# Optimization experiments

Hardware: AMD Instinct MI355X
Metric: run time of the kernel (lower is better)

Reference implementation:

```python
import jax, jax.numpy as jnp
import numpy as np

FS = 44100
N_SINES = 1000
RESAMPLE = 32
TWO_PI = 2.0 * np.pi


def _linear_upsample(x, scale):
    """Match torch F.interpolate(mode='linear', align_corners=False).
    x: [B, C, N] -> [B, C, N*scale]"""
    n = x.shape[-1]
    out_n = n * scale
    # source coordinate for each output sample
    coords = (jnp.arange(out_n, dtype=jnp.float32) + 0.5) / scale - 0.5
    coords = jnp.clip(coords, 0.0, n - 1)
    lo = jnp.floor(coords).astype(jnp.int32)
    hi = jnp.minimum(lo + 1, n - 1)
    w = (coords - lo.astype(jnp.float32)).astype(x.dtype)
    return x[..., lo] * (1.0 - w) + x[..., hi] * w


def setup_inputs() -> dict:
    key = jax.random.key(0)
    k1, k2 = jax.random.split(key)
    B, S, F = 4, N_SINES, 256
    frequencies = jax.random.uniform(k1, (B, S, F), dtype=jnp.float32) * 5000.0 + 40.0
    amplitudes = jax.random.uniform(k2, (B, S, F), dtype=jnp.float32) / N_SINES
    init_phases = jnp.zeros((B, S), dtype=jnp.float32)
    return {"frequencies": frequencies, "amplitudes": amplitudes, "init_phases": init_phases}


def reference(frequencies, amplitudes, init_phases):
    freqs = _linear_upsample(frequencies, RESAMPLE)
    amps = _linear_upsample(amplitudes, RESAMPLE)
    # angular increment per sample
    omegas = freqs * (TWO_PI / FS)
    # phase accumulation (inclusive cumsum) plus carried-in phase state
    phases = jnp.cumsum(omegas, axis=-1) + init_phases[:, :, None]
    # additive synthesis: sum over sines -> [B, 1, T]
    signal = jnp.sum(amps * jnp.sin(phases), axis=1, keepdims=True)
    return signal
```

## Files before the change

### kernel.cpp

```cpp
#include <hip/hip_runtime.h>


#define FS_D 44100.0
#define S_TOTAL 1000
#define FRAMES 256
#define T_OUT 8192
#define BATCH 4
#define CH 8
#define NC 125
#define KQ 4

template <bool ATOMIC>
__global__ __launch_bounds__(256) void synth(
    const float* __restrict__ freq, const float* __restrict__ amp,
    const float* __restrict__ initp, float* __restrict__ dst)
{
  __shared__ float base_lds[CH][FRAMES];
  __shared__ float head_lds[CH];

  const int bx    = blockIdx.x;
  const int b     = bx / (NC * KQ);
  const int rem   = bx % (NC * KQ);
  const int chunk = rem >> 2;
  const int kq    = rem & 3;
  const int s0    = chunk * CH;
  const int tid   = threadIdx.x;
  const int lane  = tid & 63;
  const int wave  = tid >> 6;

  const double inv2pi = 0.15915494309189535;
  const double k16    = 16.0 / FS_D;

  #pragma unroll
  for (int r = wave; r < CH; r += 4) {
    const int s = s0 + r;
    const long long roff = (long long)(b * S_TOTAL + s) * FRAMES;
    const float4 fv = reinterpret_cast<const float4*>(freq + roff)[lane];
    const double f0 = fv.x, f1 = fv.y, f2 = fv.z, f3 = fv.w;
    const double tot = f0 + f1 + f2 + f3;
    double incl = tot;
    #pragma unroll
    for (int off = 1; off < 64; off <<= 1) {
      double v = __shfl_up(incl, (unsigned)off, 64);
      if (lane >= off) incl += v;
    }
    double C = incl - tot;
    const double initrev = (double)initp[b * S_TOTAL + s] * inv2pi;
    if (lane == 0) head_lds[r] = (float)(initrev - floor(initrev));
    const double fk[4] = {f0, f1, f2, f3};
    #pragma unroll
    for (int i = 0; i < 4; ++i) {
      const double basev = k16 * (2.0 * C + fk[i]) + initrev;
      base_lds[r][4 * lane + i] = (float)(basev - floor(basev));
      C += fk[i];
    }
  }
  __syncthreads();

  const int g = tid >> 2;
  const int q = tid & 3;
  const int k = kq * 64 + g;
  const bool special = (k == 255);
  const bool hd      = special && (q >= 2);
  const int kA  = hd ? 0 : k;
  const int kA1 = special ? kA : (kA + 1);
  const int qq  = hd ? (q - 2) : q;
  const int j0  = qq * 8;
  const int t0  = hd ? j0 : (kA * 32 + 16 + j0);

  float uu[8], u2[8];
  const float u0f = (float)(j0 + 1);
  #pragma unroll
  for (int jj = 0; jj < 8; ++jj) {
    uu[jj] = u0f + (float)jj;
    u2[jj] = uu[jj] * uu[jj];
  }

  float acc[8];
  #pragma unroll
  for (int jj = 0; jj < 8; ++jj) acc[jj] = 0.f;

  const float invfs = (float)(1.0 / FS_D);

  #pragma unroll
  for (int r = 0; r < CH; ++r) {
    const long long roff = (long long)(b * S_TOTAL + s0 + r) * FRAMES;
    const float fA  = freq[roff + kA];
    const float fA1 = freq[roff + kA1];
    const float aA  = amp[roff + kA];
    const float aA1 = amp[roff + kA1];
    const float bs  = hd ? head_lds[r] : base_lds[r][kA];
    const float c1  = fA * invfs;
    const float c2  = (fA1 - fA) * (invfs * (1.0f / 64.0f));
    const float d1  = (aA1 - aA) * (1.0f / 32.0f);
    const float a0p = fmaf(-0.5f, d1, aA);
    #pragma unroll
    for (int jj = 0; jj < 8; ++jj) {
      const float p  = fmaf(c2, u2[jj], fmaf(c1, uu[jj], bs));
      const float am = fmaf(d1, uu[jj], a0p);
      acc[jj] = fmaf(am, __builtin_amdgcn_sinf(__builtin_amdgcn_fractf(p)), acc[jj]);
    }
  }

  if (ATOMIC) {
    float* outb = dst + (long long)b * T_OUT + t0;
    #pragma unroll
    for (int jj = 0; jj < 8; ++jj) atomicAdd(outb + jj, acc[jj]);
  } else {
    float* pout = dst + (long long)(b * NC + chunk) * T_OUT + t0;
    reinterpret_cast<float4*>(pout)[0] = make_float4(acc[0], acc[1], acc[2], acc[3]);
    reinterpret_cast<float4*>(pout)[1] = make_float4(acc[4], acc[5], acc[6], acc[7]);
  }
}

__global__ __launch_bounds__(256) void reduce_out(
    const float* __restrict__ partial, float* __restrict__ out)
{
  __shared__ float red[4][64];
  const int tid  = threadIdx.x;
  const int lane = tid & 63;
  const int w    = tid >> 6;
  const int i    = blockIdx.x * 64 + lane;
  const int b    = i >> 13;
  const int t    = i & (T_OUT - 1);
  const float* p = partial + (long long)b * NC * T_OUT + t;
  float s = 0.f;
  #pragma unroll 8
  for (int c = w; c < NC; c += 4) s += p[(long long)c * T_OUT];
  red[w][lane] = s;
  __syncthreads();
  if (tid < 64) {
    out[i] = (red[0][lane] + red[1][lane]) + (red[2][lane] + red[3][lane]);
  }
}

extern "C" void kernel_launch(void* const* d_in, const int* in_sizes, int n_in,
                              void* d_out, int out_size, void* d_ws, size_t ws_size,
                              hipStream_t stream) {
  const float* freq  = (const float*)d_in[0];
  const float* amp   = (const float*)d_in[1];
  const float* initp = (const float*)d_in[2];
  float* out = (float*)d_out;

  const size_t need = (size_t)BATCH * NC * T_OUT * sizeof(float);

  if (ws_size >= need) {
    float* partial = (float*)d_ws;
    synth<false><<<dim3(BATCH * NC * KQ), dim3(256), 0, stream>>>(
        freq, amp, initp, partial);
    reduce_out<<<dim3((BATCH * T_OUT) / 64), dim3(256), 0, stream>>>(
        partial, out);
  } else {
    hipMemsetAsync(d_out, 0, (size_t)out_size * sizeof(float), stream);
    synth<true><<<dim3(BATCH * NC * KQ), dim3(256), 0, stream>>>(
        freq, amp, initp, out);
  }
}
```

Baseline: 25.29 us.

## Store partial sums in fp16 and precompute per-frame coefficients in LDS

Partial sums written by the synth kernel become half precision, which halves the workspace traffic written by synth and read by the reduction. The reduction now reads half2 pairs and writes float2 outputs. Per-frame interpolation coefficients are computed once per block into LDS, and the thread mapping changes to wave = sub-segment, lane = frame, so redundant global loads are removed. Launch bounds now request 8 blocks per CU. Rounding partials to fp16 adds error to the output.

```diff
diff --git a/kernel.cpp b/kernel.cpp
--- a/kernel.cpp
+++ b/kernel.cpp
@@ -1,4 +1,5 @@
 #include <hip/hip_runtime.h>
+#include <hip/hip_fp16.h>
 
 
 #define FS_D 44100.0
@@ -11,12 +12,14 @@
 #define KQ 4
 
 template <bool ATOMIC>
-__global__ __launch_bounds__(256) void synth(
+__global__ __launch_bounds__(256, 8) void synth(
     const float* __restrict__ freq, const float* __restrict__ amp,
-    const float* __restrict__ initp, float* __restrict__ dst)
+    const float* __restrict__ initp, __half* __restrict__ pdst,
+    float* __restrict__ odst)
 {
   __shared__ float base_lds[CH][FRAMES];
   __shared__ float head_lds[CH];
+  __shared__ float4 coef_lds[CH][64];
 
   const int bx    = blockIdx.x;
   const int b     = bx / (NC * KQ);
@@ -28,109 +31,136 @@
   const int lane  = tid & 63;
   const int wave  = tid >> 6;
 
-  const double inv2pi = 0.15915494309189535;
-  const double k16    = 16.0 / FS_D;
+  const float invfs = (float)(1.0 / FS_D);
 
-  #pragma unroll
-  for (int r = wave; r < CH; r += 4) {
-    const int s = s0 + r;
-    const long long roff = (long long)(b * S_TOTAL + s) * FRAMES;
-    const float4 fv = reinterpret_cast<const float4*>(freq + roff)[lane];
-    const double f0 = fv.x, f1 = fv.y, f2 = fv.z, f3 = fv.w;
-    const double tot = f0 + f1 + f2 + f3;
-    double incl = tot;
+  {
+    const int kA  = kq * 64 + lane;
+    const int kA1 = (kA < FRAMES - 1) ? kA + 1 : kA;
     #pragma unroll
-    for (int off = 1; off < 64; off <<= 1) {
-      double v = __shfl_up(incl, (unsigned)off, 64);
-      if (lane >= off) incl += v;
+    for (int i = 0; i < 2; ++i) {
+      const int r = 2 * wave + i;
+      const long long roff = (long long)(b * S_TOTAL + s0 + r) * FRAMES;
+      const float fA  = freq[roff + kA];
+      const float fA1 = freq[roff + kA1];
+      const float aA  = amp[roff + kA];
+      const float aA1 = amp[roff + kA1];
+      const float c1  = fA * invfs;
+      const float c2  = (fA1 - fA) * (invfs * (1.0f / 64.0f));
+      const float d1  = (aA1 - aA) * (1.0f / 32.0f);
+      const float a0p = fmaf(-0.5f, d1, aA);
+      coef_lds[r][lane] = make_float4(c1, c2, d1, a0p);
     }
-    double C = incl - tot;
-    const double initrev = (double)initp[b * S_TOTAL + s] * inv2pi;
-    if (lane == 0) head_lds[r] = (float)(initrev - floor(initrev));
-    const double fk[4] = {f0, f1, f2, f3};
+  }
+
+  {
+    const double inv2pi = 0.15915494309189535;
+    const double k16    = 16.0 / FS_D;
     #pragma unroll
-    for (int i = 0; i < 4; ++i) {
-      const double basev = k16 * (2.0 * C + fk[i]) + initrev;
-      base_lds[r][4 * lane + i] = (float)(basev - floor(basev));
-      C += fk[i];
+    for (int r = wave; r < CH; r += 4) {
+      const int s = s0 + r;
+      const long long roff = (long long)(b * S_TOTAL + s) * FRAMES;
+      const float4 fv = reinterpret_cast<const float4*>(freq + roff)[lane];
+      const double f0 = fv.x, f1 = fv.y, f2 = fv.z, f3 = fv.w;
+      const double tot = f0 + f1 + f2 + f3;
+      double incl = tot;
+      #pragma unroll
+      for (int off = 1; off < 64; off <<= 1) {
+        double v = __shfl_up(incl, (unsigned)off, 64);
+        if (lane >= off) incl += v;
+      }
+      double C = incl - tot;
+      const double initrev = (double)initp[b * S_TOTAL + s] * inv2pi;
+      if (lane == 0) head_lds[r] = (float)(initrev - floor(initrev));
+      const double fk[4] = {f0, f1, f2, f3};
+      #pragma unroll
+      for (int i = 0; i < 4; ++i) {
+        const double basev = k16 * (2.0 * C + fk[i]) + initrev;
+        base_lds[r][4 * lane + i] = (float)(basev - floor(basev));
+        C += fk[i];
+      }
     }
   }
   __syncthreads();
 
-  const int g = tid >> 2;
-  const int q = tid & 3;
-  const int k = kq * 64 + g;
-  const bool special = (k == 255);
+  const int q = wave;
+  const int k = kq * 64 + lane;
+  const bool special = (k == FRAMES - 1);
   const bool hd      = special && (q >= 2);
-  const int kA  = hd ? 0 : k;
-  const int kA1 = special ? kA : (kA + 1);
   const int qq  = hd ? (q - 2) : q;
   const int j0  = qq * 8;
-  const int t0  = hd ? j0 : (kA * 32 + 16 + j0);
+  const int t0  = hd ? j0 : (k * 32 + 16 + j0);
 
-  float uu[8], u2[8];
+  float uu[8];
   const float u0f = (float)(j0 + 1);
   #pragma unroll
-  for (int jj = 0; jj < 8; ++jj) {
-    uu[jj] = u0f + (float)jj;
-    u2[jj] = uu[jj] * uu[jj];
-  }
+  for (int jj = 0; jj < 8; ++jj) uu[jj] = u0f + (float)jj;
 
   float acc[8];
   #pragma unroll
   for (int jj = 0; jj < 8; ++jj) acc[jj] = 0.f;
 
-  const float invfs = (float)(1.0 / FS_D);
-
   #pragma unroll
   for (int r = 0; r < CH; ++r) {
-    const long long roff = (long long)(b * S_TOTAL + s0 + r) * FRAMES;
-    const float fA  = freq[roff + kA];
-    const float fA1 = freq[roff + kA1];
-    const float aA  = amp[roff + kA];
-    const float aA1 = amp[roff + kA1];
-    const float bs  = hd ? head_lds[r] : base_lds[r][kA];
-    const float c1  = fA * invfs;
-    const float c2  = (fA1 - fA) * (invfs * (1.0f / 64.0f));
-    const float d1  = (aA1 - aA) * (1.0f / 32.0f);
-    const float a0p = fmaf(-0.5f, d1, aA);
+    float4 cf = coef_lds[r][lane];
+    float bs  = base_lds[r][k];
+    if (hd) {
+      const long long roff0 = (long long)(b * S_TOTAL + s0 + r) * FRAMES;
+      cf.x = freq[roff0] * invfs;
+      cf.y = 0.f; cf.z = 0.f;
+      cf.w = amp[roff0];
+      bs   = head_lds[r];
+    }
     #pragma unroll
     for (int jj = 0; jj < 8; ++jj) {
-      const float p  = fmaf(c2, u2[jj], fmaf(c1, uu[jj], bs));
-      const float am = fmaf(d1, uu[jj], a0p);
+      const float p  = fmaf(fmaf(cf.y, uu[jj], cf.x), uu[jj], bs);
+      const float am = fmaf(cf.z, uu[jj], cf.w);
       acc[jj] = fmaf(am, __builtin_amdgcn_sinf(__builtin_amdgcn_fractf(p)), acc[jj]);
     }
   }
 
   if (ATOMIC) {
-    float* outb = dst + (long long)b * T_OUT + t0;
+    float* outb = odst + (long long)b * T_OUT + t0;
     #pragma unroll
     for (int jj = 0; jj < 8; ++jj) atomicAdd(outb + jj, acc[jj]);
   } else {
-    float* pout = dst + (long long)(b * NC + chunk) * T_OUT + t0;
-    reinterpret_cast<float4*>(pout)[0] = make_float4(acc[0], acc[1], acc[2], acc[3]);
-    reinterpret_cast<float4*>(pout)[1] = make_float4(acc[4], acc[5], acc[6], acc[7]);
+    __half* pout = pdst + (size_t)(b * NC + chunk) * T_OUT + t0;
+    union { float4 f; __half2 h[4]; } u;
+    u.h[0] = __floats2half2_rn(acc[0], acc[1]);
+    u.h[1] = __floats2half2_rn(acc[2], acc[3]);
+    u.h[2] = __floats2half2_rn(acc[4], acc[5]);
+    u.h[3] = __floats2half2_rn(acc[6], acc[7]);
+    *reinterpret_cast<float4*>(pout) = u.f;
   }
 }
 
 __global__ __launch_bounds__(256) void reduce_out(
-    const float* __restrict__ partial, float* __restrict__ out)
+    const __half* __restrict__ partial, float* __restrict__ out)
 {
-  __shared__ float red[4][64];
+  __shared__ float red_x[4][64];
+  __shared__ float red_y[4][64];
   const int tid  = threadIdx.x;
   const int lane = tid & 63;
   const int w    = tid >> 6;
   const int i    = blockIdx.x * 64 + lane;
-  const int b    = i >> 13;
-  const int t    = i & (T_OUT - 1);
-  const float* p = partial + (long long)b * NC * T_OUT + t;
-  float s = 0.f;
+  const int b    = i >> 12;
+  const int t2   = i & 4095;
+  const __half2* p =
+      reinterpret_cast<const __half2*>(partial + (size_t)b * NC * T_OUT) + t2;
+  float sx = 0.f, sy = 0.f;
   #pragma unroll 8
-  for (int c = w; c < NC; c += 4) s += p[(long long)c * T_OUT];
-  red[w][lane] = s;
+  for (int c = w; c < NC; c += 4) {
+    const float2 v = __half22float2(p[c * (T_OUT / 2)]);
+    sx += v.x; sy += v.y;
+  }
+  red_x[w][lane] = sx;
+  red_y[w][lane] = sy;
   __syncthreads();
   if (tid < 64) {
-    out[i] = (red[0][lane] + red[1][lane]) + (red[2][lane] + red[3][lane]);
+    const float ox = (red_x[0][lane] + red_x[1][lane]) +
+                     (red_x[2][lane] + red_x[3][lane]);
+    const float oy = (red_y[0][lane] + red_y[1][lane]) +
+                     (red_y[2][lane] + red_y[3][lane]);
+    reinterpret_cast<float2*>(out)[i] = make_float2(ox, oy);
   }
 }
 
@@ -142,17 +172,17 @@
   const float* initp = (const float*)d_in[2];
   float* out = (float*)d_out;
 
-  const size_t need = (size_t)BATCH * NC * T_OUT * sizeof(float);
+  const size_t need = (size_t)BATCH * NC * T_OUT * sizeof(__half);
 
   if (ws_size >= need) {
-    float* partial = (float*)d_ws;
+    __half* partial = (__half*)d_ws;
     synth<false><<<dim3(BATCH * NC * KQ), dim3(256), 0, stream>>>(
-        freq, amp, initp, partial);
-    reduce_out<<<dim3((BATCH * T_OUT) / 64), dim3(256), 0, stream>>>(
+        freq, amp, initp, partial, nullptr);
+    reduce_out<<<dim3((BATCH * T_OUT / 2) / 64), dim3(256), 0, stream>>>(
         partial, out);
   } else {
     hipMemsetAsync(d_out, 0, (size_t)out_size * sizeof(float), stream);
     synth<true><<<dim3(BATCH * NC * KQ), dim3(256), 0, stream>>>(
-        freq, amp, initp, out);
+        freq, amp, initp, nullptr, out);
   }
 }
```

Measured after the change: 22.32 us. -11.8%, faster.
